# Optimization experiments

Measured on AMD Instinct MI355X. Metric: run time of the kernel, lower is better.

Reference implementation:

```python
import jax, jax.numpy as jnp
import numpy as np

B, L, D, H, MEM, POL = 32, 256, 768, 12, 384, 3
DK = D // H
ALPHA, BETA, GAMA = 1.0, 0.25, 0.1


def _forward(sequence_output, pooled_output, adj_reshape, src_mask, aspect_mask,
             ln_g, ln_b, wq, bq, wk, bk, wd, bd, weight_m, bias_m,
             wa0, ba0, wa1, ba1, ws0, bs0, ws1, bs1, affine1, affine2, wc, bc):
    b, l, d = sequence_output.shape
    h = weight_m.shape[0]
    dk = d // h

    # custom LayerNorm (torch std is unbiased, ddof=1)
    mu = sequence_output.mean(-1, keepdims=True)
    sd = jnp.std(sequence_output, axis=-1, keepdims=True, ddof=1)
    x = ln_g * (sequence_output - mu) / (sd + 1e-6) + ln_b  # gcn_inputs (dropout = eval identity)

    aspect_outs = x * aspect_mask[:, :, None]

    # multi-head projections  [B,H,L,dk]
    q = (x @ wq + bq).reshape(b, l, h, dk).transpose(0, 2, 1, 3)
    k = (x @ wk + bk).reshape(b, l, h, dk).transpose(0, 2, 1, 3)
    asp = aspect_outs @ wd + bd                       # [B,L,dk]
    asp = jnp.broadcast_to(asp[:, None], (b, h, l, dk))

    # aspect-conditioned scores: tanh(aspect @ W_m @ K^T + b_m)   [B,H,L,L]
    asps = jnp.tanh(jnp.einsum('bhld,hde,bhme->bhlm', asp, weight_m, k) + bias_m[0])
    avg = asps.sum(axis=-2) / l                       # [B,H,L]

    # fusion overwrite: for each aspect index idx, row idx and col idx <- avg.
    # Sequential loop semantics (ascending idx, row-then-col) collapse to:
    #   both aspect (i,j): value = avg[min(i,j)];  row-only: avg[j];  col-only: avg[i]
    is_asp = aspect_mask > 0                          # [B,L]
    rowm = is_asp[:, None, :, None]
    colm = is_asp[:, None, None, :]
    avg_i = avg[..., :, None]                         # [B,H,L,1]
    avg_j = avg[..., None, :]                         # [B,H,1,L]
    ge = (jnp.arange(l)[:, None] >= jnp.arange(l)[None, :])  # i>=j -> min=j
    both_val = jnp.where(ge, avg_j, avg_i)
    aspect_scores = jnp.where(rowm & colm, both_val,
                      jnp.where(rowm, avg_j,
                        jnp.where(colm, avg_i, asps)))

    # standard scaled-dot attention
    scores = jnp.einsum('bhld,bhmd->bhlm', q, k) / jnp.sqrt(jnp.float32(dk))
    scores = jnp.where(src_mask[:, None, None, :] == 0, -1e9, scores)
    s_attn = jax.nn.softmax(scores, axis=-1)          # dropout = eval identity

    aspect_score_avg = aspect_scores.mean(axis=1)     # [B,L,L]
    adj_s = s_attn.mean(axis=1)                       # [B,L,L]

    eye = jnp.eye(l, dtype=adj_s.dtype)
    adj_s = adj_s * (1.0 - eye) + eye                 # zero diag then add identity
    adj_s = src_mask[:, :, None] * adj_s

    adj_r = jnp.exp(ALPHA * adj_reshape)
    dist_mask = aspect_score_avg > BETA
    adj_r = jnp.where(dist_mask, 1.0, adj_r)
    adj_ag = adj_r * aspect_score_avg

    log_p = jax.nn.log_softmax(adj_ag, axis=-1)
    log_q = jax.nn.log_softmax(adj_s, axis=-1)
    q_t = jnp.exp(log_q)
    kl = jnp.sum(q_t * (log_q - log_p))
    kl_loss = jnp.exp(-1.0 * kl * GAMA)

    denom_s = adj_s.sum(axis=2, keepdims=True) + 1.0
    denom_ag = adj_ag.sum(axis=2, keepdims=True) + 1.0

    out_ag, out_s = x, x
    was = [(wa0, ba0), (wa1, ba1)]
    wss = [(ws0, bs0), (ws1, bs1)]
    for li in range(2):
        g_ag = jax.nn.relu(((adj_ag @ out_ag) @ was[li][0] + was[li][1]) / denom_ag)
        g_s = jax.nn.relu(((adj_s @ out_s) @ wss[li][0] + wss[li][1]) / denom_s)
        A1 = jax.nn.softmax(jnp.einsum('bld,de,bme->blm', g_ag, affine1, g_s), axis=-1)
        A2 = jax.nn.softmax(jnp.einsum('bld,de,bme->blm', g_s, affine2, g_ag), axis=-1)
        out_ag = A1 @ g_s
        out_s = A2 @ g_ag   # gcn_drop = eval identity

    asp_wn = aspect_mask.sum(axis=1, keepdims=True)   # [B,1]
    m = aspect_mask[:, :, None]
    outputs1 = (out_ag * m).sum(axis=1) / asp_wn      # [B,MEM]
    outputs2 = (out_s * m).sum(axis=1) / asp_wn

    final = jnp.concatenate([outputs1, outputs2, pooled_output], axis=-1) @ wc + bc
    return final, kl_loss


def setup_inputs() -> dict:
    key = jax.random.key(0)
    ks = jax.random.split(key, 16)
    s = 0.02
    pos = jnp.arange(L)
    start = 5 + (jnp.arange(B) % 16)
    aspect_mask = ((pos[None, :] >= start[:, None]) & (pos[None, :] < start[:, None] + 3)).astype(jnp.float32)
    f32 = jnp.float32
    return {
        'sequence_output': jax.random.normal(ks[0], (B, L, D), f32),
        'pooled_output': jax.random.normal(ks[1], (B, D), f32),
        'adj_reshape': jax.random.uniform(ks[2], (B, L, L), f32),
        'src_mask': jnp.ones((B, L), f32),
        'aspect_mask': aspect_mask,
        'ln_g': jnp.ones((D,), f32), 'ln_b': jnp.zeros((D,), f32),
        'wq': jax.random.normal(ks[3], (D, D), f32) * s, 'bq': jnp.zeros((D,), f32),
        'wk': jax.random.normal(ks[4], (D, D), f32) * s, 'bk': jnp.zeros((D,), f32),
        'wd': jax.random.normal(ks[5], (D, DK), f32) * s, 'bd': jnp.zeros((DK,), f32),
        'weight_m': jax.random.normal(ks[6], (H, DK, DK), f32) * s,
        'bias_m': jnp.zeros((1,), f32),
        'wa0': jax.random.normal(ks[7], (D, MEM), f32) * s, 'ba0': jnp.zeros((MEM,), f32),
        'wa1': jax.random.normal(ks[8], (MEM, MEM), f32) * s, 'ba1': jnp.zeros((MEM,), f32),
        'ws0': jax.random.normal(ks[9], (D, MEM), f32) * s, 'bs0': jnp.zeros((MEM,), f32),
        'ws1': jax.random.normal(ks[10], (MEM, MEM), f32) * s, 'bs1': jnp.zeros((MEM,), f32),
        'affine1': jax.random.normal(ks[11], (MEM, MEM), f32) * s,
        'affine2': jax.random.normal(ks[12], (MEM, MEM), f32) * s,
        'wc': jax.random.normal(ks[13], (2 * D, POL), f32) * s, 'bc': jnp.zeros((POL,), f32),
    }


def reference(sequence_output, pooled_output, adj_reshape, src_mask, aspect_mask,
              ln_g, ln_b, wq, bq, wk, bk, wd, bd, weight_m, bias_m,
              wa0, ba0, wa1, ba1, ws0, bs0, ws1, bs1, affine1, affine2, wc, bc):
    return _forward(sequence_output, pooled_output, adj_reshape, src_mask, aspect_mask,
                    ln_g, ln_b, wq, bq, wk, bk, wd, bd, weight_m, bias_m,
                    wa0, ba0, wa1, ba1, ws0, bs0, ws1, bs1, affine1, affine2, wc, bc)
```

## Files before the change

kernel.cpp:

```cpp
#include <hip/hip_runtime.h>

#define B_ 32
#define L_ 256
#define D_ 768
#define H_ 12
#define DK_ 64
#define MEM_ 384

typedef __attribute__((ext_vector_type(8))) short bfrag8;
typedef __attribute__((ext_vector_type(8))) unsigned short us8;
typedef __attribute__((ext_vector_type(4))) float f32x4;

__device__ inline unsigned short f2bf(float f) {
  unsigned u = __float_as_uint(f);
  return (unsigned short)((u + 0x7fffu + ((u >> 16) & 1u)) >> 16);
}
__device__ inline float bf2f(unsigned short u) {
  return __uint_as_float(((unsigned)u) << 16);
}
__device__ inline float tanh_fast(float x) {
  x = fminf(fmaxf(x, -30.f), 30.f);
  float e = __expf(2.f * x);
  return (e - 1.f) * __builtin_amdgcn_rcpf(e + 1.f);
}
__device__ inline void gload_lds16(const unsigned short* g, unsigned short* l) {
  __builtin_amdgcn_global_load_lds(
      (__attribute__((address_space(1))) void*)(g),
      (__attribute__((address_space(3))) void*)(l), 16, 0, 0);
}

__device__ inline float waveRedSum(float v) {
#pragma unroll
  for (int o = 32; o; o >>= 1) v += __shfl_xor(v, o, 64);
  return v;
}
__device__ inline float waveRedMax(float v) {
#pragma unroll
  for (int o = 32; o; o >>= 1) v = fmaxf(v, __shfl_xor(v, o, 64));
  return v;
}
__device__ inline float blkRedSum(float v, float* red) {
  v = waveRedSum(v);
  int w = threadIdx.x >> 6;
  __syncthreads();
  if ((threadIdx.x & 63) == 0) red[w] = v;
  __syncthreads();
  return red[0] + red[1] + red[2] + red[3];
}
__device__ inline float blkRedMax(float v, float* red) {
  v = waveRedMax(v);
  int w = threadIdx.x >> 6;
  __syncthreads();
  if ((threadIdx.x & 63) == 0) red[w] = v;
  __syncthreads();
  return fmaxf(fmaxf(red[0], red[1]), fmaxf(red[2], red[3]));
}

__global__ __launch_bounds__(256) void prep_kernel(
    const float* __restrict__ seq, const float* __restrict__ lng,
    const float* __restrict__ lnb, float* __restrict__ xout,
    unsigned short* __restrict__ xbf,
    const float* __restrict__ wq, unsigned short* __restrict__ wqT,
    const float* __restrict__ wk, unsigned short* __restrict__ wkT,
    const float* __restrict__ wa0, unsigned short* __restrict__ wa0T,
    const float* __restrict__ ws0, unsigned short* __restrict__ ws0T,
    const float* __restrict__ wa1, unsigned short* __restrict__ wa1T,
    const float* __restrict__ ws1, unsigned short* __restrict__ ws1T,
    const float* __restrict__ aff1, unsigned short* __restrict__ aff1T,
    const float* __restrict__ aff2, unsigned short* __restrict__ aff2T,
    const float* __restrict__ wd, unsigned short* __restrict__ wdT,
    const float* __restrict__ wm, unsigned short* __restrict__ wmT) {
  int bid = blockIdx.x;
  if (bid >= 600) {
    long row = bid - 600;
    const float* p = seq + row * D_;
    float v[3];
#pragma unroll
    for (int i = 0; i < 3; ++i) v[i] = p[threadIdx.x + i * 256];
    __shared__ float red[4];
    float s = v[0] + v[1] + v[2];
    s = blkRedSum(s, red);
    float mu = s * (1.f / D_);
    float ss = 0.f;
#pragma unroll
    for (int i = 0; i < 3; ++i) { float d = v[i] - mu; ss += d * d; }
    ss = blkRedSum(ss, red);
    float sd = sqrtf(ss * (1.f / (D_ - 1)));
    float inv = 1.f / (sd + 1e-6f);
#pragma unroll
    for (int i = 0; i < 3; ++i) {
      int c = threadIdx.x + i * 256;
      float o = lng[c] * (v[i] - mu) * inv + lnb[c];
      xout[row * D_ + c] = o;
      xbf[row * D_ + c] = f2bf(o);
    }
    return;
  }
  const float* src; unsigned short* dst; int Rr, Cc, tIdx;
  if (bid < 144)      { src = wq;   dst = wqT;   Rr = 768; Cc = 768; tIdx = bid; }
  else if (bid < 288) { src = wk;   dst = wkT;   Rr = 768; Cc = 768; tIdx = bid - 144; }
  else if (bid < 360) { src = wa0;  dst = wa0T;  Rr = 768; Cc = 384; tIdx = bid - 288; }
  else if (bid < 432) { src = ws0;  dst = ws0T;  Rr = 768; Cc = 384; tIdx = bid - 360; }
  else if (bid < 468) { src = wa1;  dst = wa1T;  Rr = 384; Cc = 384; tIdx = bid - 432; }
  else if (bid < 504) { src = ws1;  dst = ws1T;  Rr = 384; Cc = 384; tIdx = bid - 468; }
  else if (bid < 540) { src = aff1; dst = aff1T; Rr = 384; Cc = 384; tIdx = bid - 504; }
  else if (bid < 576) { src = aff2; dst = aff2T; Rr = 384; Cc = 384; tIdx = bid - 540; }
  else if (bid < 588) { src = wd;   dst = wdT;   Rr = 768; Cc = 64;  tIdx = bid - 576; }
  else { int h = bid - 588; src = wm + h * 4096; dst = wmT + h * 4096; Rr = 64; Cc = 64; tIdx = 0; }
  __shared__ float tile[64][65];
  int nx = Cc >> 6;
  int c0 = (tIdx % nx) * 64, r0 = (tIdx / nx) * 64;
  int tx = threadIdx.x & 63, ty = threadIdx.x >> 6;
#pragma unroll
  for (int i = 0; i < 16; ++i)
    tile[ty + i * 4][tx] = src[(long)(r0 + ty + i * 4) * Cc + c0 + tx];
  __syncthreads();
#pragma unroll
  for (int i = 0; i < 16; ++i)
    dst[(long)(c0 + ty + i * 4) * Rr + r0 + tx] = f2bf(tile[tx][ty + i * 4]);
}

template <int MR>
__global__ __launch_bounds__(256) void gemm_bb(
    const unsigned short* __restrict__ A, const unsigned short* __restrict__ Bt,
    float* __restrict__ C, unsigned short* __restrict__ Cbf,
    unsigned short* __restrict__ CT,
    int M, int N, int K, long sA, long sB, long sC, long sCT,
    const float* __restrict__ bias, const float* __restrict__ rowDiv, int relu,
    const unsigned short* __restrict__ A2, const unsigned short* __restrict__ Bt2,
    float* __restrict__ C2, unsigned short* __restrict__ Cbf2,
    unsigned short* __restrict__ CT2,
    const float* __restrict__ bias2, const float* __restrict__ rowDiv2, int zsplit) {
  constexpr int MFRAG = MR / 32;
  constexpr int RW = MR / 2;
  constexpr int ASH = MR * 32;
  constexpr int TSH = 64 * (MR + 8);
  constexpr int SMN = (ASH + 4096 > TSH) ? (ASH + 4096) : TSH;
  __shared__ alignas(16) unsigned short smem[SMN];
  unsigned short* AsS = smem;
  unsigned short* BsS = smem + ASH;
  const int tid = threadIdx.x;
  const int bn = blockIdx.x, bm = blockIdx.y;
  int bz = blockIdx.z;
  const unsigned short* Ap = A; const unsigned short* Btp = Bt;
  float* Cp = C; unsigned short* Cbp = Cbf; unsigned short* CTp = CT;
  const float* biasp = bias; const float* rowDivp = rowDiv;
  if (zsplit > 0 && bz >= zsplit) {
    bz -= zsplit;
    Ap = A2; Btp = Bt2; Cp = C2; Cbp = Cbf2; CTp = CT2; biasp = bias2; rowDivp = rowDiv2;
  }
  Ap += (long)bz * sA; Btp += (long)bz * sB;
  if (Cp) Cp += (long)bz * sC;
  if (Cbp) Cbp += (long)bz * sC;
  if (CTp) CTp += (long)bz * sCT;

  f32x4 acc[MFRAG][4] = {};
  const int l = tid & 63, w = tid >> 6;
  const int wr = w >> 1, wc = w & 1;
  const int lr = l & 15, sg = l >> 4;

  const int rc = l >> 2;
  const int sslot = (l & 3) ^ ((rc >> 1) & 3);
  const unsigned short* gA0 = Ap + (long)(bm * MR + w * 16 + rc) * K + sslot * 8;
  const unsigned short* gA1 = (MR == 128)
      ? Ap + (long)(bm * MR + (w + 4) * 16 + rc) * K + sslot * 8 : nullptr;
  const unsigned short* gB0 = Btp + (long)(bn * 128 + w * 16 + rc) * K + sslot * 8;
  const unsigned short* gB1 = Btp + (long)(bn * 128 + (w + 4) * 16 + rc) * K + sslot * 8;
  unsigned short* lA0 = AsS + w * 512;
  unsigned short* lA1 = AsS + (w + 4) * 512;
  unsigned short* lB0 = BsS + w * 512;
  unsigned short* lB1 = BsS + (w + 4) * 512;

  const int off = (sg ^ ((lr >> 1) & 3)) * 8;
  const unsigned short* arp[MFRAG];
  const unsigned short* brp[4];
#pragma unroll
  for (int m = 0; m < MFRAG; ++m)
    arp[m] = AsS + (wr * RW + m * 16 + lr) * 32 + off;
#pragma unroll
  for (int n = 0; n < 4; ++n)
    brp[n] = BsS + (wc * 64 + n * 16 + lr) * 32 + off;

  for (int k0 = 0; k0 < K; k0 += 32) {
    gload_lds16(gA0 + k0, lA0);
    if (MR == 128) gload_lds16(gA1 + k0, lA1);
    gload_lds16(gB0 + k0, lB0);
    gload_lds16(gB1 + k0, lB1);
    __syncthreads();
    bfrag8 af[MFRAG], bf[4];
#pragma unroll
    for (int m = 0; m < MFRAG; ++m) af[m] = *(const bfrag8*)(arp[m] + 0);
#pragma unroll
    for (int n = 0; n < 4; ++n) bf[n] = *(const bfrag8*)(brp[n] + 0);
#pragma unroll
    for (int m = 0; m < MFRAG; ++m)
#pragma unroll
      for (int n = 0; n < 4; ++n)
        acc[m][n] = __builtin_amdgcn_mfma_f32_16x16x32_bf16(af[m], bf[n], acc[m][n], 0, 0, 0);
    __syncthreads();
  }

  if (Cp || Cbp) {
#pragma unroll
    for (int m = 0; m < MFRAG; ++m) {
#pragma unroll
      for (int r = 0; r < 4; ++r) {
        int row = bm * MR + wr * RW + m * 16 + (l >> 4) * 4 + r;
        float rd = rowDivp ? 1.f / rowDivp[(long)bz * M + row] : 1.f;
#pragma unroll
        for (int n = 0; n < 4; ++n) {
          int col = bn * 128 + wc * 64 + n * 16 + lr;
          float v = acc[m][n][r];
          if (biasp) v += biasp[col];
          v *= rd;
          if (relu) v = fmaxf(v, 0.f);
          if (Cp) Cp[(long)row * N + col] = v;
          if (Cbp) Cbp[(long)row * N + col] = f2bf(v);
        }
      }
    }
  }
  if (CT) {
    auto Ts = (unsigned short(*)[MR + 8])smem;
#pragma unroll
    for (int ch = 0; ch < 2; ++ch) {
      __syncthreads();
      if (wc == ch) {
#pragma unroll
        for (int m = 0; m < MFRAG; ++m) {
#pragma unroll
          for (int r = 0; r < 4; ++r) {
            int rowl = wr * RW + m * 16 + (l >> 4) * 4 + r;
            float rd = rowDivp ? 1.f / rowDivp[(long)bz * M + bm * MR + rowl] : 1.f;
#pragma unroll
            for (int n = 0; n < 4; ++n) {
              int col = bn * 128 + wc * 64 + n * 16 + lr;
              float v = acc[m][n][r];
              if (biasp) v += biasp[col];
              v *= rd;
              if (relu) v = fmaxf(v, 0.f);
              Ts[n * 16 + lr][rowl] = f2bf(v);
            }
          }
        }
      }
      __syncthreads();
      int trow = tid >> 2, tc = (tid & 3) * (MR / 4);
      int colg = bn * 128 + ch * 64 + trow;
      int rowg = bm * MR + tc;
      unsigned short* dp = CTp + (long)(rowg >> 8) * sCT + (long)colg * 256 + (rowg & 255);
#pragma unroll
      for (int j = 0; j < MR / 32; ++j)
        *(us8*)(dp + j * 8) = *(const us8*)&Ts[trow][tc + j * 8];
    }
  }
}

__global__ __launch_bounds__(256) void attn_asp(
    const unsigned short* __restrict__ qbf, const unsigned short* __restrict__ kbf,
    const float* __restrict__ srcm, float* __restrict__ adj_s,
    unsigned short* __restrict__ adjsbf,
    const unsigned short* __restrict__ xbf, const unsigned short* __restrict__ wdT,
    const float* __restrict__ amask, const float* __restrict__ bd,
    unsigned short* __restrict__ aspbf) {
  int t = threadIdx.x;
  int w = t >> 6, l = t & 63;
  int lr = l & 15, kg = (l >> 4) * 8;
  if (blockIdx.x >= 512) {
    int l0 = (blockIdx.x - 512) << 4;
    const unsigned short* ap = xbf + (long)(l0 + lr) * D_ + kg;
    const unsigned short* bp = wdT + (long)(w * 16 + lr) * D_ + kg;
    f32x4 acc = {};
#pragma unroll
    for (int k0 = 0; k0 < D_; k0 += 32) {
      bfrag8 af = *(const bfrag8*)(ap + k0);
      bfrag8 bf = *(const bfrag8*)(bp + k0);
      acc = __builtin_amdgcn_mfma_f32_16x16x32_bf16(af, bf, acc, 0, 0, 0);
    }
    int col = w * 16 + lr;
#pragma unroll
    for (int r = 0; r < 4; ++r) {
      int row = l0 + (l >> 4) * 4 + r;
      float v = acc[r] * amask[row] + bd[col];
      aspbf[(long)row * DK_ + col] = f2bf(v);
    }
    return;
  }
  int blk = blockIdx.x;
  int b = blk >> 4, l0 = (blk & 15) << 4;
  int rbase = (l >> 4) * 4;
  __shared__ float red[6][2][16][8];
  float acc[4][4] = {};
  float cmv[4];
#pragma unroll
  for (int ct = 0; ct < 4; ++ct) cmv[ct] = srcm[b * L_ + w * 64 + ct * 16 + lr];

#pragma unroll 1
  for (int hp = 0; hp < 6; ++hp) {
    const unsigned short* ap = qbf + ((long)b * L_ + l0 + lr) * D_ + hp * 128 + kg;
    bfrag8 a00 = *(const bfrag8*)ap;
    bfrag8 a01 = *(const bfrag8*)(ap + 32);
    bfrag8 a10 = *(const bfrag8*)(ap + 64);
    bfrag8 a11 = *(const bfrag8*)(ap + 96);
    bfrag8 kv[4][4];
#pragma unroll
    for (int ct = 0; ct < 4; ++ct) {
      const unsigned short* bp =
          kbf + ((long)b * L_ + w * 64 + ct * 16 + lr) * D_ + hp * 128 + kg;
      kv[ct][0] = *(const bfrag8*)bp;
      kv[ct][1] = *(const bfrag8*)(bp + 32);
      kv[ct][2] = *(const bfrag8*)(bp + 64);
      kv[ct][3] = *(const bfrag8*)(bp + 96);
    }
    float sv0[4][4], sv1[4][4];
#pragma unroll
    for (int ct = 0; ct < 4; ++ct) {
      f32x4 c0 = {}, c1 = {};
      c0 = __builtin_amdgcn_mfma_f32_16x16x32_bf16(a00, kv[ct][0], c0, 0, 0, 0);
      c0 = __builtin_amdgcn_mfma_f32_16x16x32_bf16(a01, kv[ct][1], c0, 0, 0, 0);
      c1 = __builtin_amdgcn_mfma_f32_16x16x32_bf16(a10, kv[ct][2], c1, 0, 0, 0);
      c1 = __builtin_amdgcn_mfma_f32_16x16x32_bf16(a11, kv[ct][3], c1, 0, 0, 0);
      bool msk = (cmv[ct] == 0.f);
#pragma unroll
      for (int r = 0; r < 4; ++r) {
        sv0[ct][r] = msk ? -1e9f : c0[r] * 0.125f;
        sv1[ct][r] = msk ? -1e9f : c1[r] * 0.125f;
      }
    }
    float mx0a[4], mx1a[4];
#pragma unroll
    for (int r = 0; r < 4; ++r) {
      float m0 = fmaxf(fmaxf(sv0[0][r], sv0[1][r]), fmaxf(sv0[2][r], sv0[3][r]));
      float m1 = fmaxf(fmaxf(sv1[0][r], sv1[1][r]), fmaxf(sv1[2][r], sv1[3][r]));
#pragma unroll
      for (int o = 1; o < 16; o <<= 1) {
        m0 = fmaxf(m0, __shfl_xor(m0, o, 64));
        m1 = fmaxf(m1, __shfl_xor(m1, o, 64));
      }
      mx0a[r] = m0; mx1a[r] = m1;
      float s0 = 0.f, s1 = 0.f;
#pragma unroll
      for (int ct = 0; ct < 4; ++ct) {
        float e0 = __expf(sv0[ct][r] - m0);
        float e1 = __expf(sv1[ct][r] - m1);
        sv0[ct][r] = e0; sv1[ct][r] = e1;
        s0 += e0; s1 += e1;
      }
#pragma unroll
      for (int o = 1; o < 16; o <<= 1) {
        s0 += __shfl_xor(s0, o, 64);
        s1 += __shfl_xor(s1, o, 64);
      }
      if (lr == 0) {
        red[hp][0][rbase + r][w] = m0;
        red[hp][0][rbase + r][4 + w] = s0;
        red[hp][1][rbase + r][w] = m1;
        red[hp][1][rbase + r][4 + w] = s1;
      }
    }
    __syncthreads();
#pragma unroll
    for (int r = 0; r < 4; ++r) {
      f32x4 m4 = *(const f32x4*)&red[hp][0][rbase + r][0];
      f32x4 s4 = *(const f32x4*)&red[hp][0][rbase + r][4];
      float mt = fmaxf(fmaxf(m4[0], m4[1]), fmaxf(m4[2], m4[3]));
      float tot = s4[0] * __expf(m4[0] - mt) + s4[1] * __expf(m4[1] - mt) +
                  s4[2] * __expf(m4[2] - mt) + s4[3] * __expf(m4[3] - mt);
      float sc0 = __expf(mx0a[r] - mt) * __builtin_amdgcn_rcpf(tot);
      f32x4 n4 = *(const f32x4*)&red[hp][1][rbase + r][0];
      f32x4 t4 = *(const f32x4*)&red[hp][1][rbase + r][4];
      float nt = fmaxf(fmaxf(n4[0], n4[1]), fmaxf(n4[2], n4[3]));
      float tt = t4[0] * __expf(n4[0] - nt) + t4[1] * __expf(n4[1] - nt) +
                 t4[2] * __expf(n4[2] - nt) + t4[3] * __expf(n4[3] - nt);
      float sc1 = __expf(mx1a[r] - nt) * __builtin_amdgcn_rcpf(tt);
#pragma unroll
      for (int ct = 0; ct < 4; ++ct)
        acc[ct][r] += sv0[ct][r] * sc0 + sv1[ct][r] * sc1;
    }
  }

#pragma unroll
  for (int r = 0; r < 4; ++r) {
    int row = l0 + rbase + r;
    float rm = srcm[b * L_ + row];
#pragma unroll
    for (int ct = 0; ct < 4; ++ct) {
      int col = w * 64 + ct * 16 + lr;
      float v = acc[ct][r] * (1.f / H_);
      if (col == row) v = 1.f;
      v *= rm;
      long idx = ((long)b * L_ + row) * L_ + col;
      adj_s[idx] = v;
      adjsbf[idx] = f2bf(v);
    }
  }
}

__global__ __launch_bounds__(256) void asp_wm_v2(const unsigned short* __restrict__ aspbf,
                                                 const unsigned short* __restrict__ wmT,
                                                 unsigned short* __restrict__ tmpA) {
  int bh = blockIdx.x;
  int b = bh / H_, h = bh % H_;
  int t = threadIdx.x;
  int w = t >> 6, l = t & 63;
  int lr = l & 15, kg = (l >> 4) * 8;
  const unsigned short* wp = wmT + h * 4096;
  f32x4 acc[4][4] = {};
#pragma unroll
  for (int ks = 0; ks < 2; ++ks) {
    int k0 = ks * 32;
    bfrag8 af[4], bf[4];
#pragma unroll
    for (int m = 0; m < 4; ++m)
      af[m] = *(const bfrag8*)(aspbf + (long)(b * L_ + w * 64 + m * 16 + lr) * DK_ + k0 + kg);
#pragma unroll
    for (int n = 0; n < 4; ++n)
      bf[n] = *(const bfrag8*)(wp + (n * 16 + lr) * 64 + k0 + kg);
#pragma unroll
    for (int m = 0; m < 4; ++m)
#pragma unroll
      for (int n = 0; n < 4; ++n)
        acc[m][n] = __builtin_amdgcn_mfma_f32_16x16x32_bf16(af[m], bf[n], acc[m][n], 0, 0, 0);
  }
#pragma unroll
  for (int m = 0; m < 4; ++m)
#pragma unroll
    for (int n = 0; n < 4; ++n)
#pragma unroll
      for (int r = 0; r < 4; ++r) {
        int row = w * 64 + m * 16 + (l >> 4) * 4 + r;
        int col = n * 16 + lr;
        tmpA[(((long)b * H_ + h) * L_ + row) * DK_ + col] = f2bf(acc[m][n][r]);
      }
}

__global__ __launch_bounds__(256) void gemm_sfmx(
    const unsigned short* __restrict__ u1, const unsigned short* __restrict__ g1,
    unsigned short* __restrict__ P1,
    const unsigned short* __restrict__ u2, const unsigned short* __restrict__ g2,
    unsigned short* __restrict__ P2) {
  int bm = blockIdx.x;
  int bz = blockIdx.y;
  const unsigned short* Ap; const unsigned short* Bp; unsigned short* Pp;
  if (bz < 32) {
    Ap = u1 + (long)bz * L_ * MEM_; Bp = g1 + (long)bz * L_ * MEM_;
    Pp = P1 + (long)bz * L_ * L_;
  } else {
    int z = bz - 32;
    Ap = u2 + (long)z * L_ * MEM_; Bp = g2 + (long)z * L_ * MEM_;
    Pp = P2 + (long)z * L_ * L_;
  }
  __shared__ unsigned short As[64][40];
  __shared__ unsigned short Bs[256][40];
  __shared__ float redm[2][64];
  __shared__ float reds[2][64];
  const int t = threadIdx.x;
  const int l = t & 63, w = t >> 6;
  const int wr = w >> 1, wc = w & 1;
  const int lr = l & 15, kg = (l >> 4) * 8;
  f32x4 acc[2][8] = {};
  const int arA = t >> 2, akA = (t & 3) * 8;

  for (int k0 = 0; k0 < MEM_; k0 += 32) {
    *(us8*)&As[arA][akA] = *(const us8*)(Ap + (long)(bm * 64 + arA) * MEM_ + k0 + akA);
#pragma unroll
    for (int j = 0; j < 4; ++j)
      *(us8*)&Bs[t][j * 8] = *(const us8*)(Bp + (long)t * MEM_ + k0 + j * 8);
    __syncthreads();
    bfrag8 af[2], bf[8];
#pragma unroll
    for (int m = 0; m < 2; ++m) af[m] = *(const bfrag8*)&As[wr * 32 + m * 16 + lr][kg];
#pragma unroll
    for (int n = 0; n < 8; ++n) bf[n] = *(const bfrag8*)&Bs[wc * 128 + n * 16 + lr][kg];
#pragma unroll
    for (int m = 0; m < 2; ++m)
#pragma unroll
      for (int n = 0; n < 8; ++n)
        acc[m][n] = __builtin_amdgcn_mfma_f32_16x16x32_bf16(af[m], bf[n], acc[m][n], 0, 0, 0);
    __syncthreads();
  }

#pragma unroll
  for (int m = 0; m < 2; ++m) {
#pragma unroll
    for (int r = 0; r < 4; ++r) {
      int lrow = wr * 32 + m * 16 + (l >> 4) * 4 + r;
      float mx = -1e30f;
#pragma unroll
      for (int n = 0; n < 8; ++n) mx = fmaxf(mx, acc[m][n][r]);
#pragma unroll
      for (int o = 1; o < 16; o <<= 1) mx = fmaxf(mx, __shfl_xor(mx, o, 64));
      if (lr == 0) redm[wc][lrow] = mx;
    }
  }
  __syncthreads();
#pragma unroll
  for (int m = 0; m < 2; ++m) {
#pragma unroll
    for (int r = 0; r < 4; ++r) {
      int lrow = wr * 32 + m * 16 + (l >> 4) * 4 + r;
      float mx = fmaxf(redm[0][lrow], redm[1][lrow]);
      float s = 0.f;
#pragma unroll
      for (int n = 0; n < 8; ++n) {
        float e = __expf(acc[m][n][r] - mx);
        acc[m][n][r] = e;
        s += e;
      }
#pragma unroll
      for (int o = 1; o < 16; o <<= 1) s += __shfl_xor(s, o, 64);
      if (lr == 0) reds[wc][lrow] = s;
    }
  }
  __syncthreads();
#pragma unroll
  for (int m = 0; m < 2; ++m) {
#pragma unroll
    for (int r = 0; r < 4; ++r) {
      int lrow = wr * 32 + m * 16 + (l >> 4) * 4 + r;
      float inv = 1.f / (reds[0][lrow] + reds[1][lrow]);
      int row = bm * 64 + lrow;
#pragma unroll
      for (int n = 0; n < 8; ++n) {
        int col = wc * 128 + n * 16 + lr;
        Pp[(long)row * L_ + col] = f2bf(acc[m][n][r] * inv);
      }
    }
  }
}

__global__ __launch_bounds__(256) void asps_mean_v2(
    const unsigned short* __restrict__ tmpA,
    const unsigned short* __restrict__ kbf,
    const float* __restrict__ bias_m,
    float* __restrict__ asps_mean) {
  int blk = blockIdx.x;
  int b = blk >> 4, l0 = (blk & 15) << 4;
  int t = threadIdx.x;
  int w = t >> 6, l = t & 63;
  int lr = l & 15, kg = (l >> 4) * 8;
  float bm = bias_m[0];
  float accg[4][4] = {};
  for (int h = 0; h < H_; ++h) {
    const unsigned short* ap = tmpA + (((long)b * H_ + h) * L_ + l0 + lr) * 64 + kg;
    bfrag8 af0 = *(const bfrag8*)ap;
    bfrag8 af1 = *(const bfrag8*)(ap + 32);
#pragma unroll
    for (int ct = 0; ct < 4; ++ct) {
      const unsigned short* bp =
          kbf + ((long)b * L_ + w * 64 + ct * 16 + lr) * D_ + h * 64 + kg;
      bfrag8 bf0 = *(const bfrag8*)bp;
      bfrag8 bf1 = *(const bfrag8*)(bp + 32);
      f32x4 accl = {};
      accl = __builtin_amdgcn_mfma_f32_16x16x32_bf16(af0, bf0, accl, 0, 0, 0);
      accl = __builtin_amdgcn_mfma_f32_16x16x32_bf16(af1, bf1, accl, 0, 0, 0);
#pragma unroll
      for (int r = 0; r < 4; ++r) accg[ct][r] += tanh_fast(accl[r] + bm);
    }
  }
#pragma unroll
  for (int ct = 0; ct < 4; ++ct) {
    int col = w * 64 + ct * 16 + lr;
#pragma unroll
    for (int r = 0; r < 4; ++r) {
      int row = l0 + (l >> 4) * 4 + r;
      asps_mean[((long)b * L_ + row) * L_ + col] = accg[ct][r] * (1.f / H_);
    }
  }
}

__global__ __launch_bounds__(1024) void avgh_kernel(const float* __restrict__ asps_mean,
                                                    float* __restrict__ avgH) {
  int b = blockIdx.x;
  int m = threadIdx.x & 255, q = threadIdx.x >> 8;
  __shared__ float part[4][256];
  float s = 0.f;
  for (int l = q * 64; l < q * 64 + 64; ++l)
    s += asps_mean[((long)b * L_ + l) * L_ + m];
  part[q][m] = s;
  __syncthreads();
  if (q == 0)
    avgH[b * L_ + m] = (part[0][m] + part[1][m] + part[2][m] + part[3][m]) * (1.f / L_);
}

__global__ __launch_bounds__(256) void adjag_kl(const float* __restrict__ asps_mean,
                                                const float* __restrict__ avgH,
                                                const float* __restrict__ amask,
                                                const float* __restrict__ adjr,
                                                const float* __restrict__ adj_s,
                                                float* __restrict__ adj_ag,
                                                unsigned short* __restrict__ adjagbf,
                                                float* __restrict__ klpart,
                                                float* __restrict__ den_s,
                                                float* __restrict__ den_ag) {
  long row = blockIdx.x;
  int m = threadIdx.x;
  int l = (int)(row & 255);
  int b = (int)(row >> 8);
  long idx = row * L_ + m;
  bool rowa = amask[b * L_ + l] > 0.f;
  bool cola = amask[b * L_ + m] > 0.f;
  float asa;
  if (rowa && cola) asa = (l >= m) ? avgH[b * L_ + m] : avgH[b * L_ + l];
  else if (rowa)    asa = avgH[b * L_ + m];
  else if (cola)    asa = avgH[b * L_ + l];
  else              asa = asps_mean[idx];
  float r = (asa > 0.25f) ? 1.f : expf(adjr[idx]);
  float a = r * asa;
  adj_ag[idx] = a;
  adjagbf[idx] = f2bf(a);

  __shared__ float red[4];
  float s = adj_s[idx];
  float sum_s = blkRedSum(s, red);
  float sum_a = blkRedSum(a, red);
  float mx_s = blkRedMax(s, red);
  float mx_a = blkRedMax(a, red);
  float es = expf(s - mx_s), ea = expf(a - mx_a);
  float ses = blkRedSum(es, red);
  float sea = blkRedSum(ea, red);
  float logq = (s - mx_s) - logf(ses);
  float logp = (a - mx_a) - logf(sea);
  float term = (es / ses) * (logq - logp);
  float kp = blkRedSum(term, red);
  if (m == 0) {
    klpart[row] = kp;
    den_s[row] = sum_s + 1.f;
    den_ag[row] = sum_a + 1.f;
  }
}

__global__ __launch_bounds__(256) void final_kernel(const unsigned short* __restrict__ o_ag,
                                                    const unsigned short* __restrict__ o_s,
                                                    const float* __restrict__ pooled,
                                                    const float* __restrict__ amask,
                                                    const float* __restrict__ wc,
                                                    const float* __restrict__ bc,
                                                    const float* __restrict__ klpart,
                                                    float* __restrict__ dout) {
  int b = blockIdx.x, t = threadIdx.x;
  __shared__ float red[4];
  if (b == B_) {
    float s = 0.f;
    for (int i = t; i < B_ * L_; i += 256) s += klpart[i];
    s = blkRedSum(s, red);
    if (t == 0) dout[96] = expf(-s * 0.1f);
    return;
  }
  __shared__ float cS[1536];
  __shared__ float maskS[256];
  maskS[t] = amask[b * L_ + t];
  float wn = blkRedSum(maskS[t], red);
  for (int e = t; e < MEM_; e += 256) {
    float s1 = 0.f, s2 = 0.f;
    for (int l = 0; l < L_; ++l) {
      float mk = maskS[l];
      if (mk != 0.f) {
        s1 += mk * bf2f(o_ag[((long)b * L_ + l) * MEM_ + e]);
        s2 += mk * bf2f(o_s[((long)b * L_ + l) * MEM_ + e]);
      }
    }
    cS[e] = s1 / wn;
    cS[MEM_ + e] = s2 / wn;
  }
  for (int j = t; j < D_; j += 256) cS[2 * MEM_ + j] = pooled[b * D_ + j];
  __syncthreads();
  float p0 = 0.f, p1 = 0.f, p2 = 0.f;
  for (int j = t; j < 1536; j += 256) {
    float v = cS[j];
    p0 += v * wc[j * 3 + 0];
    p1 += v * wc[j * 3 + 1];
    p2 += v * wc[j * 3 + 2];
  }
  p0 = blkRedSum(p0, red);
  p1 = blkRedSum(p1, red);
  p2 = blkRedSum(p2, red);
  if (t == 0) {
    dout[b * 3 + 0] = p0 + bc[0];
    dout[b * 3 + 1] = p1 + bc[1];
    dout[b * 3 + 2] = p2 + bc[2];
  }
}

extern "C" void kernel_launch(void* const* d_in, const int* in_sizes, int n_in,
                              void* d_out, int out_size, void* d_ws, size_t ws_size,
                              hipStream_t stream) {
  const float* seq    = (const float*)d_in[0];
  const float* pooled = (const float*)d_in[1];
  const float* adjr   = (const float*)d_in[2];
  const float* srcm   = (const float*)d_in[3];
  const float* amask  = (const float*)d_in[4];
  const float* ln_g   = (const float*)d_in[5];
  const float* ln_b   = (const float*)d_in[6];
  const float* wq     = (const float*)d_in[7];
  const float* bq     = (const float*)d_in[8];
  const float* wk     = (const float*)d_in[9];
  const float* bk     = (const float*)d_in[10];
  const float* wd     = (const float*)d_in[11];
  const float* bd     = (const float*)d_in[12];
  const float* wm     = (const float*)d_in[13];
  const float* bm     = (const float*)d_in[14];
  const float* wa0    = (const float*)d_in[15];
  const float* ba0    = (const float*)d_in[16];
  const float* wa1    = (const float*)d_in[17];
  const float* ba1    = (const float*)d_in[18];
  const float* ws0    = (const float*)d_in[19];
  const float* bs0    = (const float*)d_in[20];
  const float* ws1    = (const float*)d_in[21];
  const float* bs1    = (const float*)d_in[22];
  const float* aff1   = (const float*)d_in[23];
  const float* aff2   = (const float*)d_in[24];
  const float* wc     = (const float*)d_in[25];
  const float* bc     = (const float*)d_in[26];

  float* ws = (float*)d_ws;
  float* S0 = ws;
  float* S1 = S0 + 6291456;
  float* S2 = S1 + 3145728;
  float* S3 = S2 + 3145728;
  float* S4 = S3 + 3145728;
  float* S5 = S4 + 524288;
  float* adj_s  = S5 + 2097152;
  float* adj_ag = adj_s + 2097152;
  unsigned short* adjsbf  = (unsigned short*)(adj_ag + 2097152);
  unsigned short* adjagbf = adjsbf + 2097152;
  unsigned short* wT      = adjagbf + 2097152;
  unsigned short* wqT   = wT;
  unsigned short* wkT   = wT + 589824;
  unsigned short* wa0T  = wT + 1179648;
  unsigned short* ws0T  = wT + 1474560;
  unsigned short* wa1T  = wT + 1769472;
  unsigned short* ws1T  = wT + 1916928;
  unsigned short* aff1T = wT + 2064384;
  unsigned short* aff2T = wT + 2211840;
  float* tail   = (float*)(wT + 2359296);
  float* avgH   = tail;
  float* den_s  = avgH + 8192;
  float* den_ag = den_s + 8192;
  float* klp    = den_ag + 8192;

  float* x = S0;
  unsigned short* o_agbf = (unsigned short*)S0;
  unsigned short* o_sbf  = o_agbf + 3145728;
  unsigned short* gTag   = o_agbf + 6291456;
  unsigned short* gTs    = o_agbf + 9437184;
  unsigned short* xbf    = (unsigned short*)S1;
  unsigned short* qbf    = (unsigned short*)S2;
  unsigned short* tmpA   = (unsigned short*)S2;
  unsigned short* g_agbf = (unsigned short*)S2;
  unsigned short* g_sbf  = g_agbf + 3145728;
  unsigned short* kbf    = (unsigned short*)S3;
  unsigned short* tTag   = (unsigned short*)S3;
  unsigned short* tTs    = tTag + 3145728;
  unsigned short* u1bf   = (unsigned short*)S3;
  unsigned short* u2bf   = u1bf + 3145728;
  unsigned short* aspbf  = (unsigned short*)S4;
  unsigned short* wdT    = aspbf + 524288;
  unsigned short* wmT    = wdT + 49152;
  float* asps = S5;
  unsigned short* P1bf = (unsigned short*)S5;
  unsigned short* P2bf = P1bf + 2097152;
  float* dout = (float*)d_out;

  const long sAdjSh = (long)L_ * L_;
  const long sMemSh = (long)L_ * MEM_;

  prep_kernel<<<600 + B_ * L_, 256, 0, stream>>>(
      seq, ln_g, ln_b, x, xbf, wq, wqT, wk, wkT, wa0, wa0T, ws0, ws0T,
      wa1, wa1T, ws1, ws1T, aff1, aff1T, aff2, aff2T, wd, wdT, wm, wmT);
  gemm_bb<64><<<dim3(6, 128, 2), 256, 0, stream>>>(
      xbf, wqT, nullptr, qbf, nullptr, 8192, 768, 768, 0, 0, 0, 0, bq, nullptr, 0,
      xbf, wkT, nullptr, kbf, nullptr, bk, nullptr, 1);
  attn_asp<<<1024, 256, 0, stream>>>(qbf, kbf, srcm, adj_s, adjsbf,
                                     xbf, wdT, amask, bd, aspbf);
  asp_wm_v2<<<B_ * H_, 256, 0, stream>>>(aspbf, wmT, tmpA);
  asps_mean_v2<<<B_ * 16, 256, 0, stream>>>(tmpA, kbf, bm, asps);
  avgh_kernel<<<B_, 1024, 0, stream>>>(asps, avgH);
  adjag_kl<<<B_ * L_, 256, 0, stream>>>(asps, avgH, amask, adjr, adj_s,
                                        adj_ag, adjagbf, klp, den_s, den_ag);

  for (int li = 0; li < 2; ++li) {
    int Kd = li ? MEM_ : D_;
    const unsigned short* inag = li ? o_agbf : xbf;
    const unsigned short* ins  = li ? o_sbf : xbf;
    const unsigned short* wAT = li ? wa1T : wa0T;
    const float* bA = li ? ba1 : ba0;
    const unsigned short* wST = li ? ws1T : ws0T;
    const float* bS = li ? bs1 : bs0;
    gemm_bb<64><<<dim3(3, 128, 2), 256, 0, stream>>>(
        inag, wAT, nullptr, nullptr, tTag, 8192, MEM_, Kd, 0, 0, 0, sMemSh,
        nullptr, nullptr, 0,
        ins, wST, nullptr, nullptr, tTs, nullptr, nullptr, 1);
    gemm_bb<64><<<dim3(3, 4, 64), 256, 0, stream>>>(
        adjagbf, tTag, nullptr, g_agbf, gTag, L_, MEM_, L_, sAdjSh, sMemSh, sMemSh,
        sMemSh, bA, den_ag, 1,
        adjsbf, tTs, nullptr, g_sbf, gTs, bS, den_s, 32);
    gemm_bb<64><<<dim3(3, 128, 2), 256, 0, stream>>>(
        g_agbf, aff1T, nullptr, u1bf, nullptr, 8192, MEM_, MEM_, 0, 0, 0, 0,
        nullptr, nullptr, 0,
        g_sbf, aff2T, nullptr, u2bf, nullptr, nullptr, nullptr, 1);
    gemm_sfmx<<<dim3(4, 64), 256, 0, stream>>>(u1bf, g_sbf, P1bf, u2bf, g_agbf, P2bf);
    gemm_bb<64><<<dim3(3, 4, 64), 256, 0, stream>>>(
        P1bf, gTs, nullptr, o_agbf, nullptr, L_, MEM_, L_, sAdjSh, sMemSh, sMemSh, 0,
        nullptr, nullptr, 0,
        P2bf, gTag, nullptr, o_sbf, nullptr, nullptr, nullptr, 32);
  }

  final_kernel<<<B_ + 1, 256, 0, stream>>>(o_agbf, o_sbf, pooled, amask, wc, bc,
                                           klp, dout);
}
```

Baseline: 429.1 us.

## Double-buffer LDS tiles in bf16 GEMM and use larger row tiles for QK projection

The GEMM k-loop now uses two LDS buffers. Loads for the next 32-wide k-slice are issued before computing on the current slice, which removes one barrier per iteration and overlaps global-to-LDS traffic with MFMA work. The Q/K projection launch switches from 64-row to 128-row tiles, halving the grid and increasing reuse of the B tiles. Doubling LDS use may reduce occupancy.

```diff
diff --git a/kernel.cpp b/kernel.cpp
--- a/kernel.cpp
+++ b/kernel.cpp
@@ -134,11 +134,10 @@
   constexpr int MFRAG = MR / 32;
   constexpr int RW = MR / 2;
   constexpr int ASH = MR * 32;
+  constexpr int BUFS = ASH + 4096;
   constexpr int TSH = 64 * (MR + 8);
-  constexpr int SMN = (ASH + 4096 > TSH) ? (ASH + 4096) : TSH;
+  constexpr int SMN = (2 * BUFS > TSH) ? 2 * BUFS : TSH;
   __shared__ alignas(16) unsigned short smem[SMN];
-  unsigned short* AsS = smem;
-  unsigned short* BsS = smem + ASH;
   const int tid = threadIdx.x;
   const int bn = blockIdx.x, bm = blockIdx.y;
   int bz = blockIdx.z;
@@ -166,32 +165,38 @@
       ? Ap + (long)(bm * MR + (w + 4) * 16 + rc) * K + sslot * 8 : nullptr;
   const unsigned short* gB0 = Btp + (long)(bn * 128 + w * 16 + rc) * K + sslot * 8;
   const unsigned short* gB1 = Btp + (long)(bn * 128 + (w + 4) * 16 + rc) * K + sslot * 8;
-  unsigned short* lA0 = AsS + w * 512;
-  unsigned short* lA1 = AsS + (w + 4) * 512;
-  unsigned short* lB0 = BsS + w * 512;
-  unsigned short* lB1 = BsS + (w + 4) * 512;
-
-  const int off = (sg ^ ((lr >> 1) & 3)) * 8;
-  const unsigned short* arp[MFRAG];
-  const unsigned short* brp[4];
-#pragma unroll
-  for (int m = 0; m < MFRAG; ++m)
-    arp[m] = AsS + (wr * RW + m * 16 + lr) * 32 + off;
-#pragma unroll
-  for (int n = 0; n < 4; ++n)
-    brp[n] = BsS + (wc * 64 + n * 16 + lr) * 32 + off;
-
-  for (int k0 = 0; k0 < K; k0 += 32) {
-    gload_lds16(gA0 + k0, lA0);
-    if (MR == 128) gload_lds16(gA1 + k0, lA1);
-    gload_lds16(gB0 + k0, lB0);
-    gload_lds16(gB1 + k0, lB1);
-    __syncthreads();
+  const int stA0 = w * 512, stA1 = (w + 4) * 512;
+  const int stB0 = ASH + w * 512, stB1 = ASH + (w + 4) * 512;
+
+  const int swz = (sg ^ ((lr >> 1) & 3)) * 8;
+  int aoff[MFRAG], boff[4];
+#pragma unroll
+  for (int m = 0; m < MFRAG; ++m) aoff[m] = (wr * RW + m * 16 + lr) * 32 + swz;
+#pragma unroll
+  for (int n = 0; n < 4; ++n) boff[n] = ASH + (wc * 64 + n * 16 + lr) * 32 + swz;
+
+  const int nt = K >> 5;
+  gload_lds16(gA0, smem + stA0);
+  if (MR == 128) gload_lds16(gA1, smem + stA1);
+  gload_lds16(gB0, smem + stB0);
+  gload_lds16(gB1, smem + stB1);
+  __syncthreads();
+
+  for (int t = 0; t < nt; ++t) {
+    const int cur = (t & 1) * BUFS;
+    if (t + 1 < nt) {
+      const int nxt = ((t + 1) & 1) * BUFS;
+      const int k1 = (t + 1) << 5;
+      gload_lds16(gA0 + k1, smem + nxt + stA0);
+      if (MR == 128) gload_lds16(gA1 + k1, smem + nxt + stA1);
+      gload_lds16(gB0 + k1, smem + nxt + stB0);
+      gload_lds16(gB1 + k1, smem + nxt + stB1);
+    }
     bfrag8 af[MFRAG], bf[4];
 #pragma unroll
-    for (int m = 0; m < MFRAG; ++m) af[m] = *(const bfrag8*)(arp[m] + 0);
-#pragma unroll
-    for (int n = 0; n < 4; ++n) bf[n] = *(const bfrag8*)(brp[n] + 0);
+    for (int m = 0; m < MFRAG; ++m) af[m] = *(const bfrag8*)(smem + cur + aoff[m]);
+#pragma unroll
+    for (int n = 0; n < 4; ++n) bf[n] = *(const bfrag8*)(smem + cur + boff[n]);
 #pragma unroll
     for (int m = 0; m < MFRAG; ++m)
 #pragma unroll
@@ -768,7 +773,7 @@
   prep_kernel<<<600 + B_ * L_, 256, 0, stream>>>(
       seq, ln_g, ln_b, x, xbf, wq, wqT, wk, wkT, wa0, wa0T, ws0, ws0T,
       wa1, wa1T, ws1, ws1T, aff1, aff1T, aff2, aff2T, wd, wdT, wm, wmT);
-  gemm_bb<64><<<dim3(6, 128, 2), 256, 0, stream>>>(
+  gemm_bb<128><<<dim3(6, 64, 2), 256, 0, stream>>>(
       xbf, wqT, nullptr, qbf, nullptr, 8192, 768, 768, 0, 0, 0, 0, bq, nullptr, 0,
       xbf, wkT, nullptr, kbf, nullptr, bk, nullptr, 1);
   attn_asp<<<1024, 256, 0, stream>>>(qbf, kbf, srcm, adj_s, adjsbf,
```

After: 408.0 us. -4.9%, faster.
